# Performance work log

Hardware: AMD Instinct MI355X
Metric: run time of the kernel (lower is better)

Reference implementation:

```python
import jax, jax.numpy as jnp
import numpy as np

B, C, N = 8, 2048, 512

def setup_inputs() -> dict:
    key = jax.random.key(0)
    ks = jax.random.split(key, 7)
    s = 1.0 / np.sqrt(N)
    return {
        "x":  jax.random.normal(ks[0], (B, C, N), dtype=jnp.float32),
        "Wq": jax.random.normal(ks[1], (N, N), dtype=jnp.float32) * s,
        "bq": jax.random.normal(ks[2], (N,), dtype=jnp.float32) * 0.01,
        "Wk": jax.random.normal(ks[3], (N, N), dtype=jnp.float32) * s,
        "bk": jax.random.normal(ks[4], (N,), dtype=jnp.float32) * 0.01,
        "Wv": jax.random.normal(ks[5], (N, N), dtype=jnp.float32) * s,
        "bv": jax.random.normal(ks[6], (N,), dtype=jnp.float32) * 0.01,
    }

def reference(x, Wq, bq, Wk, bk, Wv, bv):
    b, c, n = x.shape
    # QKV projections (torch Linear: x @ W.T + b)
    q = jnp.einsum('bcn,mn->bcm', x, Wq) + bq
    k = jnp.einsum('bcn,mn->bcm', x, Wk) + bk
    v = jnp.einsum('bcn,mn->bcm', x, Wv) + bv
    # attention over the C (token) dim: [b, c, c]
    attn = jnp.einsum('bcn,bdn->bcd', q, k)
    attn = jax.nn.softmax(attn, axis=-1) / jnp.sqrt(jnp.float32(n))
    # dropout is identity in eval mode
    out = jnp.einsum('bcd,bdn->bcn', attn, v)  # [b, c, n]
    # faithful to torch: .transpose(1, 2).reshape(B, C, N)
    score = jnp.transpose(out, (0, 2, 1)).reshape(b, c, n)
    return score
```

## Files before the change

### kernel.cpp

```cpp
#include <hip/hip_runtime.h>


typedef _Float16 half_t;
typedef __attribute__((ext_vector_type(8))) _Float16 half8;
typedef __attribute__((ext_vector_type(4))) _Float16 half4;
typedef __attribute__((ext_vector_type(4))) float    f32x4;

#define MFMA16x32(A_, B_, C_) __builtin_amdgcn_mfma_f32_16x16x32_f16((A_), (B_), (C_), 0, 0, 0)

__device__ __forceinline__ void gload_lds16(const void* g, void* l) {
  __builtin_amdgcn_global_load_lds(
      (const __attribute__((address_space(1))) void*)g,
      (__attribute__((address_space(3))) void*)l, 16, 0, 0);
}

__device__ __forceinline__ float dpp_max16(float x) {
  int t;
  t = __builtin_amdgcn_update_dpp(__float_as_int(x), __float_as_int(x), 0xB1, 0xF, 0xF, false);
  x = fmaxf(x, __int_as_float(t));
  t = __builtin_amdgcn_update_dpp(__float_as_int(x), __float_as_int(x), 0x4E, 0xF, 0xF, false);
  x = fmaxf(x, __int_as_float(t));
  t = __builtin_amdgcn_update_dpp(__float_as_int(x), __float_as_int(x), 0x124, 0xF, 0xF, false);
  x = fmaxf(x, __int_as_float(t));
  t = __builtin_amdgcn_update_dpp(__float_as_int(x), __float_as_int(x), 0x128, 0xF, 0xF, false);
  x = fmaxf(x, __int_as_float(t));
  return x;
}
__device__ __forceinline__ float dpp_sum16(float x) {
  int t;
  t = __builtin_amdgcn_update_dpp(__float_as_int(x), __float_as_int(x), 0xB1, 0xF, 0xF, false);
  x += __int_as_float(t);
  t = __builtin_amdgcn_update_dpp(__float_as_int(x), __float_as_int(x), 0x4E, 0xF, 0xF, false);
  x += __int_as_float(t);
  t = __builtin_amdgcn_update_dpp(__float_as_int(x), __float_as_int(x), 0x124, 0xF, 0xF, false);
  x += __int_as_float(t);
  t = __builtin_amdgcn_update_dpp(__float_as_int(x), __float_as_int(x), 0x128, 0xF, 0xF, false);
  x += __int_as_float(t);
  return x;
}

__global__ void cast_all(const float* __restrict__ x, const float* __restrict__ Wq,
                         const float* __restrict__ Wk, const float* __restrict__ Wv,
                         half_t* __restrict__ xh, half_t* __restrict__ wqh,
                         half_t* __restrict__ wkh, half_t* __restrict__ wvh) {
  int idx = blockIdx.x * 256 + threadIdx.x;
  const float* s;
  half_t* d;
  int off;
  if (idx < 2097152) { s = x; d = xh; off = idx; }
  else {
    int w = idx - 2097152;
    int which = w >> 16;
    off = w & 65535;
    s = (which == 0) ? Wq : (which == 1) ? Wk : Wv;
    d = (which == 0) ? wqh : (which == 1) ? wkh : wvh;
  }
  f32x4 v = ((const f32x4*)s)[off];
  half4 h;
#pragma unroll
  for (int j = 0; j < 4; ++j) h[j] = (_Float16)v[j];
  *(half4*)&d[(size_t)off * 4] = h;
}

template <int NKT, int SA, int SB, int MR>
__device__ __forceinline__ void gemm_core(
    const char* Abytes, const char* Bbytes,
    half_t* At, half_t* Bt, int tid, f32x4 (&acc)[MR][4]) {
  const int lane = tid & 63;
  const int wv = tid >> 6;
  const int g = lane >> 4, li = lane & 15;
  const int wm = wv >> 1, wn = wv & 1;
  const int ASTRIDE = MR * 2048;

  auto STAGE = [&](int kc, int buf) {
#pragma unroll
    for (int i2 = 0; i2 < MR; ++i2) {
      int seg = i2 * 256 + tid;
      int row = seg >> 3, blk = seg & 7;
      int bsrc = blk ^ (row & 7);
      gload_lds16(Abytes + ((size_t)row * SA + kc + bsrc * 8) * 2,
                  (void*)&At[buf * ASTRIDE + seg * 8]);
    }
#pragma unroll
    for (int i2 = 0; i2 < 4; ++i2) {
      int seg = i2 * 256 + tid;
      int row = seg >> 3, blk = seg & 7;
      int bsrc = blk ^ (row & 7);
      gload_lds16(Bbytes + ((size_t)row * SB + kc + bsrc * 8) * 2,
                  (void*)&Bt[buf * 8192 + seg * 8]);
    }
  };

  STAGE(0, 0);
  __syncthreads();
  int cur = 0;
#pragma unroll 1
  for (int kt = 0; kt < NKT; ++kt) {
    if (kt + 1 < NKT) STAGE((kt + 1) * 64, cur ^ 1);
#pragma unroll
    for (int kk = 0; kk < 2; ++kk) {
      half8 af[MR], bf[4];
#pragma unroll
      for (int i = 0; i < MR; ++i) {
        int ar = wm * (MR * 16) + i * 16 + li;
        af[i] = *(const half8*)&At[cur * ASTRIDE + ar * 64 + (((4 * kk + g) ^ (ar & 7)) * 8)];
      }
#pragma unroll
      for (int j = 0; j < 4; ++j) {
        int br = wn * 64 + j * 16 + li;
        bf[j] = *(const half8*)&Bt[cur * 8192 + br * 64 + (((4 * kk + g) ^ (br & 7)) * 8)];
      }
#pragma unroll
      for (int i = 0; i < MR; ++i)
#pragma unroll
        for (int j = 0; j < 4; ++j) acc[i][j] = MFMA16x32(af[i], bf[j], acc[i][j]);
    }
    __syncthreads();
    cur ^= 1;
  }
}

template <int MODE>
__global__ __launch_bounds__(256) void proj_gemm(
    const half_t* __restrict__ A, const half_t* __restrict__ Bm,
    const float* __restrict__ bias, half_t* __restrict__ out) {
  __shared__ half_t At[2 * 4 * 2048];
  __shared__ half_t Bt[2 * 8192];
  const int tid = threadIdx.x;
  const int lane = tid & 63, wv = tid >> 6;
  const int g = lane >> 4, li = lane & 15;
  const int wm = wv >> 1, wn = wv & 1;
  const int M0 = blockIdx.x * 128, N0 = blockIdx.y * 128;

  const f32x4 kZero = {0.f, 0.f, 0.f, 0.f};
  f32x4 acc[4][4];
#pragma unroll
  for (int i = 0; i < 4; ++i)
#pragma unroll
    for (int j = 0; j < 4; ++j) acc[i][j] = kZero;

  gemm_core<8, 512, 512, 4>((const char*)(A + (size_t)M0 * 512),
                            (const char*)(Bm + (size_t)N0 * 512), At, Bt, tid, acc);

  if (MODE == 2) {
#pragma unroll
    for (int i = 0; i < 4; ++i) {
      int trow = M0 + wm * 64 + i * 16 + 4 * g;
#pragma unroll
      for (int j = 0; j < 4; ++j) {
        int m = N0 + wn * 64 + j * 16 + li;
        float bs = bias[m];
#pragma unroll
        for (int r = 0; r < 4; ++r) {
          out[(size_t)(trow + r) * 512 + m] = (_Float16)(acc[i][j][r] + bs);
        }
      }
    }
  } else {
#pragma unroll
    for (int i = 0; i < 4; ++i) {
      int m0r = M0 + wm * 64 + i * 16 + 4 * g;
#pragma unroll
      for (int r = 0; r < 4; ++r) {
        int m = m0r + r;
        float bs = bias[m];
#pragma unroll
        for (int j = 0; j < 4; ++j) {
          int t = N0 + wn * 64 + j * 16 + li;
          out[(size_t)m * 16384 + t] = (_Float16)(acc[i][j][r] + bs);
        }
      }
    }
  }
}

__global__ __launch_bounds__(256) void s_pmax(
    const half_t* __restrict__ q, const half_t* __restrict__ k,
    half_t* __restrict__ Pp, float* __restrict__ m_t, float* __restrict__ l_t) {
  __shared__ half_t At[2 * 2 * 2048];
  __shared__ half_t Bt[2 * 8192];
  __shared__ float  mx2[2][64];
  __shared__ float  sm2[2][64];
  const int tid = threadIdx.x;
  const int lane = tid & 63, wv = tid >> 6;
  const int g = lane >> 4, li = lane & 15;
  const int wm = wv >> 1, wn = wv & 1;
  const int id = blockIdx.x;
  const int b = id & 7;
  const int idx = id >> 3;
  const int M0 = (idx & 31) * 64;
  const int N0 = (idx >> 5) * 128;
  const int tile = idx >> 5;

  const f32x4 kZero = {0.f, 0.f, 0.f, 0.f};
  f32x4 acc[2][4];
#pragma unroll
  for (int i = 0; i < 2; ++i)
#pragma unroll
    for (int j = 0; j < 4; ++j) acc[i][j] = kZero;

  gemm_core<8, 512, 512, 2>(
      (const char*)(q + (size_t)(b * 2048 + M0) * 512),
      (const char*)(k + (size_t)(b * 2048 + N0) * 512), At, Bt, tid, acc);

  float lmax[2][4];
#pragma unroll
  for (int i = 0; i < 2; ++i)
#pragma unroll
    for (int r = 0; r < 4; ++r) {
      float v = fmaxf(fmaxf(acc[0 + i][0][r], acc[i][1][r]),
                      fmaxf(acc[i][2][r], acc[i][3][r]));
      lmax[i][r] = dpp_max16(v);
    }
  if (li == 0) {
#pragma unroll
    for (int i = 0; i < 2; ++i)
#pragma unroll
      for (int r = 0; r < 4; ++r)
        mx2[wn][wm * 32 + i * 16 + 4 * g + r] = lmax[i][r];
  }
  __syncthreads();

  const size_t grow0 = (size_t)(b * 2048 + M0 + wm * 32);
  float tsum[2][4];
#pragma unroll
  for (int i = 0; i < 2; ++i) {
#pragma unroll
    for (int r = 0; r < 4; ++r) {
      int lr = wm * 32 + i * 16 + 4 * g + r;
      float m = fmaxf(mx2[0][lr], mx2[1][lr]);
      float s = 0.f;
#pragma unroll
      for (int j = 0; j < 4; ++j) {
        float p = __expf(acc[i][j][r] - m);
        s += p;
        Pp[(grow0 + i * 16 + 4 * g + r) * 2048 + N0 + wn * 64 + j * 16 + li] =
            (_Float16)p;
      }
      tsum[i][r] = dpp_sum16(s);
      lmax[i][r] = m;
    }
  }
  if (li == 0) {
#pragma unroll
    for (int i = 0; i < 2; ++i)
#pragma unroll
      for (int r = 0; r < 4; ++r)
        sm2[wn][wm * 32 + i * 16 + 4 * g + r] = tsum[i][r];
  }
  __syncthreads();
  if (wn == 0 && li == 0) {
#pragma unroll
    for (int i = 0; i < 2; ++i)
#pragma unroll
      for (int r = 0; r < 4; ++r) {
        int lr = wm * 32 + i * 16 + 4 * g + r;
        m_t[(grow0 + i * 16 + 4 * g + r) * 16 + tile] = lmax[i][r];
        l_t[(grow0 + i * 16 + 4 * g + r) * 16 + tile] = sm2[0][lr] + sm2[1][lr];
      }
  }
}

__global__ void sm_merge(const float* __restrict__ m_t, const float* __restrict__ l_t,
                         float* __restrict__ sc_g, float* __restrict__ l_fin) {
  int rr = blockIdx.x * 256 + threadIdx.x;
  float m[16];
  float mg = -3e38f;
#pragma unroll
  for (int t = 0; t < 16; ++t) { m[t] = m_t[rr * 16 + t]; mg = fmaxf(mg, m[t]); }
  float l = 0.f;
#pragma unroll
  for (int t = 0; t < 16; ++t) {
    float s = __expf(m[t] - mg);
    sc_g[rr * 16 + t] = s;
    l += l_t[rr * 16 + t] * s;
  }
  l_fin[rr] = l;
}

__global__ __launch_bounds__(256) void pv_gemm(
    const half_t* __restrict__ Pp, const half_t* __restrict__ vt,
    const float* __restrict__ sc_g, const float* __restrict__ l_fin,
    float* __restrict__ outp) {
  __shared__ half_t At[2][2 * 2048];
  __shared__ half_t Bt[2][8192];
  __shared__ float  sc[64][17];
  const int tid = threadIdx.x;
  const int lane = tid & 63, wv = tid >> 6;
  const int g = lane >> 4, li = lane & 15;
  const int wm = wv >> 1, wn = wv & 1;
  const int id = blockIdx.x;
  const int b = id & 7;
  const int idx = id >> 3;
  const int M0 = (idx >> 2) * 64;
  const int N0 = (idx & 3) * 128;
  const int rgb = b * 2048 + M0;

#pragma unroll
  for (int i2 = 0; i2 < 4; ++i2) {
    int e = i2 * 256 + tid;
    int row = e >> 4, t = e & 15;
    sc[row][t] = sc_g[(size_t)(rgb + row) * 16 + t];
  }

  const half_t* Pb = Pp + (size_t)rgb * 2048;
  const char* Bb = (const char*)(vt + (size_t)N0 * 16384 + (size_t)b * 2048);

  auto BSTAGE = [&](int kt, int buf) {
#pragma unroll
    for (int i2 = 0; i2 < 4; ++i2) {
      int seg = i2 * 256 + tid;
      int row = seg >> 3, blk = seg & 7;
      int bsrc = blk ^ (row & 7);
      gload_lds16(Bb + ((size_t)row * 16384 + kt * 64 + bsrc * 8) * 2,
                  (void*)&Bt[buf][seg * 8]);
    }
  };
  const int s0row = tid >> 3, s0blk = tid & 7;
  const int s1row = (256 + tid) >> 3, s1blk = tid & 7;

  __syncthreads();

  half8 a0 = *(const half8*)&Pb[(size_t)s0row * 2048 + s0blk * 8];
  half8 a1 = *(const half8*)&Pb[(size_t)s1row * 2048 + s1blk * 8];
  BSTAGE(0, 0);
  {
    _Float16 f0 = (_Float16)sc[s0row][0], f1 = (_Float16)sc[s1row][0];
#pragma unroll
    for (int e = 0; e < 8; ++e) { a0[e] *= f0; a1[e] *= f1; }
    *(half8*)&At[0][s0row * 64 + ((s0blk ^ (s0row & 7)) * 8)] = a0;
    *(half8*)&At[0][s1row * 64 + ((s1blk ^ (s1row & 7)) * 8)] = a1;
  }
  __syncthreads();

  const f32x4 kZero = {0.f, 0.f, 0.f, 0.f};
  f32x4 acc[2][4];
#pragma unroll
  for (int i = 0; i < 2; ++i)
#pragma unroll
    for (int j = 0; j < 4; ++j) acc[i][j] = kZero;

  int cur = 0;
#pragma unroll 1
  for (int kt = 0; kt < 32; ++kt) {
    half8 n0, n1;
    if (kt + 1 < 32) {
      n0 = *(const half8*)&Pb[(size_t)s0row * 2048 + (kt + 1) * 64 + s0blk * 8];
      n1 = *(const half8*)&Pb[(size_t)s1row * 2048 + (kt + 1) * 64 + s1blk * 8];
      BSTAGE(kt + 1, cur ^ 1);
    }
#pragma unroll
    for (int kk = 0; kk < 2; ++kk) {
      half8 af[2], bf[4];
#pragma unroll
      for (int i = 0; i < 2; ++i) {
        int arr = wm * 32 + i * 16 + li;
        af[i] = *(const half8*)&At[cur][arr * 64 + (((4 * kk + g) ^ (arr & 7)) * 8)];
      }
#pragma unroll
      for (int j = 0; j < 4; ++j) {
        int br = wn * 64 + j * 16 + li;
        bf[j] = *(const half8*)&Bt[cur][br * 64 + (((4 * kk + g) ^ (br & 7)) * 8)];
      }
#pragma unroll
      for (int i = 0; i < 2; ++i)
#pragma unroll
        for (int j = 0; j < 4; ++j) acc[i][j] = MFMA16x32(af[i], bf[j], acc[i][j]);
    }
    if (kt + 1 < 32) {
      _Float16 f0 = (_Float16)sc[s0row][(kt + 1) >> 1];
      _Float16 f1 = (_Float16)sc[s1row][(kt + 1) >> 1];
#pragma unroll
      for (int e = 0; e < 8; ++e) { n0[e] *= f0; n1[e] *= f1; }
      *(half8*)&At[cur ^ 1][s0row * 64 + ((s0blk ^ (s0row & 7)) * 8)] = n0;
      *(half8*)&At[cur ^ 1][s1row * 64 + ((s1blk ^ (s1row & 7)) * 8)] = n1;
    }
    __syncthreads();
    cur ^= 1;
  }

#pragma unroll
  for (int i = 0; i < 2; ++i) {
    int c0r = M0 + wm * 32 + i * 16 + 4 * g;
    float inv[4];
#pragma unroll
    for (int r = 0; r < 4; ++r)
      inv[r] = 1.0f / (l_fin[b * 2048 + c0r + r] * 22.62741699796952f);
#pragma unroll
    for (int j = 0; j < 4; ++j) {
      int n = N0 + wn * 64 + j * 16 + li;
      float* ob = outp + (size_t)b * 1048576 + (size_t)n * 2048 + c0r;
#pragma unroll
      for (int r = 0; r < 4; ++r) {
        ob[r] = acc[i][j][r] * inv[r];
      }
    }
  }
}

extern "C" void kernel_launch(void* const* d_in, const int* in_sizes, int n_in,
                              void* d_out, int out_size, void* d_ws, size_t ws_size,
                              hipStream_t stream) {
  const float* x  = (const float*)d_in[0];
  const float* Wq = (const float*)d_in[1];
  const float* bq = (const float*)d_in[2];
  const float* Wk = (const float*)d_in[3];
  const float* bk = (const float*)d_in[4];
  const float* Wv = (const float*)d_in[5];
  const float* bv = (const float*)d_in[6];

  half_t* qsb  = (half_t*)d_ws;
  half_t* ksb  = qsb + (size_t)16384 * 512;
  half_t* vtb  = ksb + (size_t)16384 * 512;
  half_t* Pp   = vtb + (size_t)512 * 16384;
  half_t* xh   = Pp;
  half_t* wqh  = xh  + (size_t)16384 * 512;
  half_t* wkh  = wqh + (size_t)512 * 512;
  half_t* wvh  = wkh + (size_t)512 * 512;
  float*  m_t  = (float*)(Pp + (size_t)16384 * 2048);
  float*  l_t  = m_t + (size_t)16384 * 16;
  float*  sc_g = l_t + (size_t)16384 * 16;
  float*  l_fin = sc_g + (size_t)16384 * 16;

  cast_all<<<dim3(8960), 256, 0, stream>>>(x, Wq, Wk, Wv, xh, wqh, wkh, wvh);

  proj_gemm<2><<<dim3(128, 4), 256, 0, stream>>>(xh, wqh, bq, qsb);
  proj_gemm<2><<<dim3(128, 4), 256, 0, stream>>>(xh, wkh, bk, ksb);
  proj_gemm<1><<<dim3(4, 128), 256, 0, stream>>>(wvh, xh, bv, vtb);

  s_pmax<<<dim3(4096), 256, 0, stream>>>(qsb, ksb, Pp, m_t, l_t);
  sm_merge<<<dim3(64), 256, 0, stream>>>(m_t, l_t, sc_g, l_fin);
  pv_gemm<<<dim3(1024), 256, 0, stream>>>(Pp, vtb, sc_g, l_fin, (float*)d_out);
}
```

Before: 177.7 us.

## Load P tiles directly to LDS and apply tile rescale in fp32 accumulators

The PV GEMM previously loaded P through registers, scaled each half8 by the per-tile softmax correction factor, and stored it into LDS. Now P is fetched asynchronously with global_load_lds like V, and the correction is applied once per 128-column group by accumulating into temporary fp32 accumulators, then folding them into the main accumulators with the scale. This removes register staging and fp16 multiplies from the inner loop and lets the A loads overlap like the B loads. The cost is extra accumulator registers and a per-group FMA pass. It also moves the scaling from fp16 to fp32, which slightly changes numerics.

```diff
diff --git a/kernel.cpp b/kernel.cpp
--- a/kernel.cpp
+++ b/kernel.cpp
@@ -208,7 +208,7 @@
   for (int i = 0; i < 2; ++i)
 #pragma unroll
     for (int r = 0; r < 4; ++r) {
-      float v = fmaxf(fmaxf(acc[0 + i][0][r], acc[i][1][r]),
+      float v = fmaxf(fmaxf(acc[i][0][r], acc[i][1][r]),
                       fmaxf(acc[i][2][r], acc[i][3][r]));
       lmax[i][r] = dpp_max16(v);
     }
@@ -282,7 +282,7 @@
     const half_t* __restrict__ Pp, const half_t* __restrict__ vt,
     const float* __restrict__ sc_g, const float* __restrict__ l_fin,
     float* __restrict__ outp) {
-  __shared__ half_t At[2][2 * 2048];
+  __shared__ half_t At[2][4096];
   __shared__ half_t Bt[2][8192];
   __shared__ float  sc[64][17];
   const int tid = threadIdx.x;
@@ -303,10 +303,18 @@
     sc[row][t] = sc_g[(size_t)(rgb + row) * 16 + t];
   }
 
-  const half_t* Pb = Pp + (size_t)rgb * 2048;
+  const char* Ab = (const char*)(Pp + (size_t)rgb * 2048);
   const char* Bb = (const char*)(vt + (size_t)N0 * 16384 + (size_t)b * 2048);
 
-  auto BSTAGE = [&](int kt, int buf) {
+  auto STAGE = [&](int kt, int buf) {
+#pragma unroll
+    for (int i2 = 0; i2 < 2; ++i2) {
+      int seg = i2 * 256 + tid;
+      int row = seg >> 3, blk = seg & 7;
+      int bsrc = blk ^ (row & 7);
+      gload_lds16(Ab + ((size_t)row * 2048 + kt * 64 + bsrc * 8) * 2,
+                  (void*)&At[buf][seg * 8]);
+    }
 #pragma unroll
     for (int i2 = 0; i2 < 4; ++i2) {
       int seg = i2 * 256 + tid;
@@ -316,21 +324,8 @@
                   (void*)&Bt[buf][seg * 8]);
     }
   };
-  const int s0row = tid >> 3, s0blk = tid & 7;
-  const int s1row = (256 + tid) >> 3, s1blk = tid & 7;
-
-  __syncthreads();
-
-  half8 a0 = *(const half8*)&Pb[(size_t)s0row * 2048 + s0blk * 8];
-  half8 a1 = *(const half8*)&Pb[(size_t)s1row * 2048 + s1blk * 8];
-  BSTAGE(0, 0);
-  {
-    _Float16 f0 = (_Float16)sc[s0row][0], f1 = (_Float16)sc[s1row][0];
-#pragma unroll
-    for (int e = 0; e < 8; ++e) { a0[e] *= f0; a1[e] *= f1; }
-    *(half8*)&At[0][s0row * 64 + ((s0blk ^ (s0row & 7)) * 8)] = a0;
-    *(half8*)&At[0][s1row * 64 + ((s1blk ^ (s1row & 7)) * 8)] = a1;
-  }
+
+  STAGE(0, 0);
   __syncthreads();
 
   const f32x4 kZero = {0.f, 0.f, 0.f, 0.f};
@@ -342,41 +337,48 @@
 
   int cur = 0;
 #pragma unroll 1
-  for (int kt = 0; kt < 32; ++kt) {
-    half8 n0, n1;
-    if (kt + 1 < 32) {
-      n0 = *(const half8*)&Pb[(size_t)s0row * 2048 + (kt + 1) * 64 + s0blk * 8];
-      n1 = *(const half8*)&Pb[(size_t)s1row * 2048 + (kt + 1) * 64 + s1blk * 8];
-      BSTAGE(kt + 1, cur ^ 1);
-    }
-#pragma unroll
-    for (int kk = 0; kk < 2; ++kk) {
-      half8 af[2], bf[4];
-#pragma unroll
-      for (int i = 0; i < 2; ++i) {
-        int arr = wm * 32 + i * 16 + li;
-        af[i] = *(const half8*)&At[cur][arr * 64 + (((4 * kk + g) ^ (arr & 7)) * 8)];
-      }
-#pragma unroll
-      for (int j = 0; j < 4; ++j) {
-        int br = wn * 64 + j * 16 + li;
-        bf[j] = *(const half8*)&Bt[cur][br * 64 + (((4 * kk + g) ^ (br & 7)) * 8)];
-      }
-#pragma unroll
-      for (int i = 0; i < 2; ++i)
-#pragma unroll
-        for (int j = 0; j < 4; ++j) acc[i][j] = MFMA16x32(af[i], bf[j], acc[i][j]);
-    }
-    if (kt + 1 < 32) {
-      _Float16 f0 = (_Float16)sc[s0row][(kt + 1) >> 1];
-      _Float16 f1 = (_Float16)sc[s1row][(kt + 1) >> 1];
-#pragma unroll
-      for (int e = 0; e < 8; ++e) { n0[e] *= f0; n1[e] *= f1; }
-      *(half8*)&At[cur ^ 1][s0row * 64 + ((s0blk ^ (s0row & 7)) * 8)] = n0;
-      *(half8*)&At[cur ^ 1][s1row * 64 + ((s1blk ^ (s1row & 7)) * 8)] = n1;
-    }
-    __syncthreads();
-    cur ^= 1;
+  for (int t16 = 0; t16 < 16; ++t16) {
+    f32x4 tmp[2][4];
+#pragma unroll
+    for (int i = 0; i < 2; ++i)
+#pragma unroll
+      for (int j = 0; j < 4; ++j) tmp[i][j] = kZero;
+
+#pragma unroll
+    for (int hh = 0; hh < 2; ++hh) {
+      int kt = t16 * 2 + hh;
+      if (kt + 1 < 32) STAGE(kt + 1, cur ^ 1);
+#pragma unroll
+      for (int kk = 0; kk < 2; ++kk) {
+        half8 af[2], bf[4];
+#pragma unroll
+        for (int i = 0; i < 2; ++i) {
+          int ar = wm * 32 + i * 16 + li;
+          af[i] = *(const half8*)&At[cur][ar * 64 + (((4 * kk + g) ^ (ar & 7)) * 8)];
+        }
+#pragma unroll
+        for (int j = 0; j < 4; ++j) {
+          int br = wn * 64 + j * 16 + li;
+          bf[j] = *(const half8*)&Bt[cur][br * 64 + (((4 * kk + g) ^ (br & 7)) * 8)];
+        }
+#pragma unroll
+        for (int i = 0; i < 2; ++i)
+#pragma unroll
+          for (int j = 0; j < 4; ++j) tmp[i][j] = MFMA16x32(af[i], bf[j], tmp[i][j]);
+      }
+      __syncthreads();
+      cur ^= 1;
+    }
+
+#pragma unroll
+    for (int i = 0; i < 2; ++i) {
+#pragma unroll
+      for (int r = 0; r < 4; ++r) {
+        float s = sc[wm * 32 + i * 16 + 4 * g + r][t16];
+#pragma unroll
+        for (int j = 0; j < 4; ++j) acc[i][j][r] += s * tmp[i][j][r];
+      }
+    }
   }
 
 #pragma unroll
```

New measurement: 179.1 us. About the same (+0.8%).
